# Kernel optimization log

Hardware: AMD Instinct MI355X
Metric: run time of the kernel (lower is better)

Reference implementation:

```python
import jax, jax.numpy as jnp
import numpy as np

N_SAMPLES = 16384
L = 8000   # num pseudo labels
C = 8      # num cameras
D = 256    # feature dim
N = 512    # batch size
T = 0.05   # temperature
K = 50     # hard_neg_k
LW = 0.5   # inter-cam loss weight


def setup_inputs() -> dict:
    key = jax.random.key(0)
    k1, k2, k3, k4, k5 = jax.random.split(key, 5)
    feats = jax.random.normal(k1, (N, D), dtype=jnp.float32)
    indexes = jax.random.randint(k2, (N,), 0, N_SAMPLES)
    label_table = jax.random.randint(k3, (N_SAMPLES,), 0, L)
    cam_table = jax.random.randint(k4, (N_SAMPLES,), 0, C)
    centers = jax.random.normal(k5, (L * C, D), dtype=jnp.float32)
    centers = centers / jnp.linalg.norm(centers, axis=1, keepdims=True)
    return {"feats": feats, "indexes": indexes, "label_table": label_table,
            "cam_table": cam_table, "centers": centers}


def reference(feats, indexes, label_table, cam_table, centers):
    # F.normalize(feats, p=2, dim=1)
    feats = feats / jnp.linalg.norm(feats, axis=1, keepdims=True)
    labels = label_table[indexes]          # [n]
    cams = cam_table[indexes]              # [n]
    cen = jax.lax.stop_gradient(centers)   # centers are a non-grad buffer in torch

    all_sims = feats @ cen.T               # [n, P]  P = L*C, proxy(l,c) = l*C + c
    n, P = all_sims.shape
    sims_r = all_sims.reshape(n, L, C)     # [n, L, C]

    # ---- intra-camera loss: softmax over the L proxies sharing sample's camera ----
    idx_cam = jnp.broadcast_to(cams[:, None, None], (n, L, 1))
    sims_intra = jnp.take_along_axis(sims_r, idx_cam, axis=2)[..., 0]  # [n, L]
    logp_intra = jax.nn.log_softmax(sims_intra / T, axis=1)
    loss_intra_i = -jnp.take_along_axis(logp_intra, labels[:, None], axis=1)[:, 0]

    # ---- inter-camera loss: C positives (same label, all cams) + top-K hard negatives ----
    idx_lab = jnp.broadcast_to(labels[:, None, None], (n, 1, C))
    pos_sims = jnp.take_along_axis(sims_r, idx_lab, axis=1)[:, 0, :]   # [n, C]
    masked = jnp.where(jnp.arange(L)[None, :, None] == labels[:, None, None],
                       jnp.float32(-10000.0), sims_r).reshape(n, P)
    neg_sims, _ = jax.lax.top_k(masked, K)                             # [n, K]
    logits = jnp.concatenate([pos_sims, neg_sims], axis=1) / T         # [n, C+K]
    logp = jax.nn.log_softmax(logits, axis=1)
    loss_inter_i = -jnp.mean(logp[:, :C], axis=1)  # target = 1/C on the C positives

    # ---- per-camera mean, summed over cameras (matches the torch.unique loop) ----
    ones = jnp.ones((n,), feats.dtype)
    counts = jax.ops.segment_sum(ones, cams, num_segments=C)
    safe = jnp.maximum(counts, 1.0)
    s_intra = jax.ops.segment_sum(loss_intra_i, cams, num_segments=C)
    s_inter = jax.ops.segment_sum(loss_inter_i, cams, num_segments=C)
    loss_intra = jnp.sum(jnp.where(counts > 0, s_intra / safe, 0.0))
    loss_inter = LW * jnp.sum(jnp.where(counts > 0, s_inter / safe, 0.0))
    return jnp.stack([loss_intra, loss_inter])
```

## Files before the change

kernel.cpp:

```cpp
#include <hip/hip_runtime.h>
#include <stdint.h>

#define NS   512
#define DDIM 256
#define LL   8000
#define CC   8
#define PP   64000
#define KTOP 50
#define CAP  1024
#define BC   64
#define NBLK (PP/BC)
#define K2C  28.853900817779268f

typedef float f32x4 __attribute__((ext_vector_type(4)));
typedef short bf16x8 __attribute__((ext_vector_type(8)));

__device__ __forceinline__ ushort f2bf(float x) {
    uint32_t b = __float_as_uint(x);
    b += 0x7fffu + ((b >> 16) & 1u);
    return (ushort)(b >> 16);
}
__device__ __forceinline__ float bf2f(ushort u) {
    return __uint_as_float(((uint32_t)u) << 16);
}

__global__ void k_norm_gather(const float* __restrict__ feats,
                              const int* __restrict__ indexes,
                              const int* __restrict__ ltab,
                              const int* __restrict__ ctab,
                              ushort* __restrict__ feats_b,
                              int* __restrict__ labels,
                              int* __restrict__ cams,
                              int* __restrict__ gcount) {
    const int n = blockIdx.x;
    const int lane = threadIdx.x;
    f32x4 v = ((const f32x4*)(feats + (size_t)n * DDIM))[lane];
    float ss = v[0]*v[0] + v[1]*v[1] + v[2]*v[2] + v[3]*v[3];
#pragma unroll
    for (int off = 32; off > 0; off >>= 1) ss += __shfl_down(ss, off);
    float tot = __shfl(ss, 0);
    float sc = 1.0f / sqrtf(tot);
    ushort4 o;
    o.x = f2bf(v[0] * sc); o.y = f2bf(v[1] * sc);
    o.z = f2bf(v[2] * sc); o.w = f2bf(v[3] * sc);
    ((ushort4*)(feats_b + (size_t)n * DDIM))[lane] = o;
    if (lane == 0) {
        int idx = indexes[n];
        labels[n] = ltab[idx];
        cams[n] = ctab[idx];
        gcount[n] = 0;
    }
}

__global__ __launch_bounds__(256, 2)
void k_gemm_fused(const ushort* __restrict__ A, const float* __restrict__ B,
                  const int* __restrict__ labels, const int* __restrict__ cams,
                  float* __restrict__ partial, float* __restrict__ cand,
                  int* __restrict__ gcount, float* __restrict__ posbuf) {
    const int bx    = blockIdx.x;
    const int cBase = bx * BC;
    const int gBase = cBase >> 3;
    const int tid   = threadIdx.x;
    const int lane  = tid & 63;
    const int w     = tid >> 6;
    const int lr    = lane & 15;
    const int lk    = lane >> 4;

    __shared__ ushort sB[BC][264];
    __shared__ int    s_lab[NS];
    __shared__ int    s_cam[NS];
    __shared__ float  s_intra[NS];
    __shared__ float  s_redA[256];
    __shared__ float  s_redB[256];
    __shared__ float  s_tau;

#pragma unroll
    for (int it = 0; it < 16; ++it) {
        int q   = tid + it * 256;
        int col = q >> 6;
        int k4  = q & 63;
        f32x4 a = *(const f32x4*)(B + (size_t)(cBase + col) * DDIM + k4 * 4);
        ushort4 o;
        o.x = f2bf(a[0]); o.y = f2bf(a[1]); o.z = f2bf(a[2]); o.w = f2bf(a[3]);
        *(ushort4*)(&sB[col][k4 * 4]) = o;
    }
    for (int r = tid; r < NS; r += 256) {
        s_lab[r] = labels[r];
        s_cam[r] = cams[r];
        s_intra[r] = 0.0f;
    }
    __syncthreads();

    const ushort* Abase = A + (size_t)(w * 128) * DDIM;
    bf16x8 acur[8];
#pragma unroll
    for (int m = 0; m < 8; ++m)
        acur[m] = *(const bf16x8*)(Abase + (size_t)(m * 16 + lr) * DDIM + lk * 8);

    f32x4 zero = {0.f, 0.f, 0.f, 0.f};
    f32x4 acc[8][4];
#pragma unroll
    for (int m = 0; m < 8; ++m)
#pragma unroll
        for (int nn = 0; nn < 4; ++nn) acc[m][nn] = zero;

#pragma unroll
    for (int kb = 0; kb < 8; ++kb) {
        const int kpos = kb * 32 + lk * 8;
        bf16x8 bfr[4];
#pragma unroll
        for (int nn = 0; nn < 4; ++nn)
            bfr[nn] = *(const bf16x8*)(&sB[nn * 16 + lr][kpos]);
        bf16x8 anxt[8];
        if (kb < 7) {
#pragma unroll
            for (int m = 0; m < 8; ++m)
                anxt[m] = *(const bf16x8*)(Abase + (size_t)(m * 16 + lr) * DDIM + kpos + 32);
        }
#pragma unroll
        for (int m = 0; m < 8; ++m)
#pragma unroll
            for (int nn = 0; nn < 4; ++nn)
                acc[m][nn] = __builtin_amdgcn_mfma_f32_16x16x32_bf16(acur[m], bfr[nn], acc[m][nn], 0, 0, 0);
        if (kb < 7) {
#pragma unroll
            for (int m = 0; m < 8; ++m) acur[m] = anxt[m];
        }
    }

    float ss = 0.0f, sc2 = 0.0f;
#pragma unroll
    for (int m = 0; m < 8; ++m)
#pragma unroll
        for (int nn = 0; nn < 4; ++nn)
#pragma unroll
            for (int j = 0; j < 4; ++j) {
                float v = acc[m][nn][j];
                if (fabsf(v) < 0.25f) { ss += v * v; sc2 += 1.0f; }
            }
    s_redA[tid] = ss; s_redB[tid] = sc2;
    __syncthreads();
    for (int off = 128; off > 0; off >>= 1) {
        if (tid < off) { s_redA[tid] += s_redA[tid + off]; s_redB[tid] += s_redB[tid + off]; }
        __syncthreads();
    }
    if (tid == 0) s_tau = 2.9f * sqrtf(s_redA[0] / fmaxf(s_redB[0], 1.0f));
    __syncthreads();
    const float tau = s_tau;

#pragma unroll
    for (int m = 0; m < 8; ++m) {
#pragma unroll
        for (int j = 0; j < 4; ++j) {
            const int r   = w * 128 + m * 16 + lk * 4 + j;
            const int lab = s_lab[r];
            const int cm  = s_cam[r];
            const bool mycam  = ((lr & 7) == cm);
            const bool hasLab = ((unsigned)(lab - gBase) < 8u);
            float isum = 0.0f;
#pragma unroll
            for (int nn = 0; nn < 4; ++nn) {
                const float v = acc[m][nn][j];
                if (mycam) isum += exp2f(v * K2C);
                const int g = gBase + ((nn * 16 + lr) >> 3);
                if (hasLab && g == lab) {
                    posbuf[r * CC + (lr & 7)] = v;
                } else if (v > tau) {
                    int id = atomicAdd(&gcount[r], 1);
                    if (id < CAP) cand[(size_t)r * CAP + id] = v;
                }
            }
            if (mycam) atomicAdd(&s_intra[r], isum);
        }
    }
    __syncthreads();
    for (int r = tid; r < NS; r += 256)
        partial[(size_t)bx * NS + r] = s_intra[r];
}

__global__ __launch_bounds__(256)
void k_row(const ushort* __restrict__ fb, const float* __restrict__ B,
           const float* __restrict__ partial, const float* __restrict__ cand,
           const int* __restrict__ gcount, const float* __restrict__ posbuf,
           const int* __restrict__ labels, const int* __restrict__ cams,
           float* __restrict__ li, float* __restrict__ le) {
    const int n = blockIdx.x;
    const int tid = threadIdx.x;
    __shared__ float red[256];
    __shared__ int   redi[256];
    __shared__ float spos[CC];
    __shared__ float scand[CAP];
    __shared__ float f[DDIM];
    __shared__ float s_lo, s_hi;
    __shared__ int   s_done, s_cnt;

    float s = 0.0f;
    for (int b = tid; b < NBLK; b += 256) s += partial[(size_t)b * NS + n];
    red[tid] = s;
    __syncthreads();
    for (int off = 128; off > 0; off >>= 1) {
        if (tid < off) red[tid] += red[tid + off];
        __syncthreads();
    }
    if (tid < CC) spos[tid] = posbuf[n * CC + tid];
    __syncthreads();
    if (tid == 0) li[n] = logf(red[0]) - 20.0f * spos[cams[n]];

    int c = gcount[n];
    if (c >= KTOP && c <= CAP) {
        for (int i = tid; i < c; i += 256) scand[i] = cand[(size_t)n * CAP + i];
    } else {
        if (tid < DDIM) f[tid] = bf2f(fb[(size_t)n * DDIM + tid]);
        const int label = labels[n];
        if (tid == 0) { s_lo = -1.01f; s_hi = 1.01f; s_done = 0; s_cnt = 0; }
        __syncthreads();
        for (int it = 0; it < 16; ++it) {
            if (s_done) break;
            float tm = 0.5f * (s_lo + s_hi);
            int cnt = 0;
            for (int p = tid; p < PP; p += 256) {
                if ((p >> 3) == label) continue;
                const float* col = B + (size_t)p * DDIM;
                float d = 0.0f;
                for (int k = 0; k < DDIM; ++k) d += f[k] * bf2f(f2bf(col[k]));
                cnt += (d > tm);
            }
            redi[tid] = cnt;
            __syncthreads();
            for (int off = 128; off > 0; off >>= 1) {
                if (tid < off) redi[tid] += redi[tid + off];
                __syncthreads();
            }
            int tot = redi[0];
            __syncthreads();
            if (tot >= KTOP && tot <= CAP) {
                if (tid == 0) s_cnt = 0;
                __syncthreads();
                for (int p = tid; p < PP; p += 256) {
                    if ((p >> 3) == label) continue;
                    const float* col = B + (size_t)p * DDIM;
                    float d = 0.0f;
                    for (int k = 0; k < DDIM; ++k) d += f[k] * bf2f(f2bf(col[k]));
                    if (d > tm) {
                        int id = atomicAdd(&s_cnt, 1);
                        if (id < CAP) scand[id] = d;
                    }
                }
                __syncthreads();
                if (tid == 0) s_done = 1;
            } else {
                if (tid == 0) { if (tot < KTOP) s_hi = tm; else s_lo = tm; }
            }
            __syncthreads();
        }
        if (!s_done) {
            if (tid == 0) s_cnt = 0;
            __syncthreads();
            float tl = s_lo;
            for (int p = tid; p < PP; p += 256) {
                if ((p >> 3) == label) continue;
                const float* col = B + (size_t)p * DDIM;
                float d = 0.0f;
                for (int k = 0; k < DDIM; ++k) d += f[k] * bf2f(f2bf(col[k]));
                if (d > tl) {
                    int id = atomicAdd(&s_cnt, 1);
                    if (id < CAP) scand[id] = d;
                }
            }
        }
        __syncthreads();
        c = s_cnt;
        if (c > CAP) c = CAP;
    }
    __syncthreads();

    float sum = 0.0f;
    for (int i = tid; i < c; i += 256) {
        float v = scand[i];
        int rk = 0;
        for (int j = 0; j < c; ++j) {
            float u = scand[j];
            rk += (u > v) || (u == v && j < i);
        }
        if (rk < KTOP) sum += exp2f(v * K2C);
    }
    if (tid < CC) sum += exp2f(spos[tid] * K2C);
    red[tid] = sum;
    __syncthreads();
    for (int off = 128; off > 0; off >>= 1) {
        if (tid < off) red[tid] += red[tid + off];
        __syncthreads();
    }
    if (tid == 0) {
        float ps = 0.0f;
#pragma unroll
        for (int j = 0; j < CC; ++j) ps += spos[j];
        le[n] = logf(red[0]) - 2.5f * ps;
    }
}

__global__ void k_finalize(const float* __restrict__ li, const float* __restrict__ le,
                           const int* __restrict__ cams, float* __restrict__ out) {
    __shared__ float si[CC], se[CC];
    __shared__ int sc[CC];
    int tid = threadIdx.x;
    if (tid < CC) { si[tid] = 0.f; se[tid] = 0.f; sc[tid] = 0; }
    __syncthreads();
    for (int i = tid; i < NS; i += 256) {
        int cm = cams[i];
        atomicAdd(&si[cm], li[i]);
        atomicAdd(&se[cm], le[i]);
        atomicAdd(&sc[cm], 1);
    }
    __syncthreads();
    if (tid == 0) {
        float a = 0.f, b = 0.f;
        for (int cm = 0; cm < CC; ++cm) {
            if (sc[cm] > 0) {
                a += si[cm] / (float)sc[cm];
                b += se[cm] / (float)sc[cm];
            }
        }
        out[0] = a;
        out[1] = 0.5f * b;
    }
}

extern "C" void kernel_launch(void* const* d_in, const int* in_sizes, int n_in,
                              void* d_out, int out_size, void* d_ws, size_t ws_size,
                              hipStream_t stream) {
    const float* feats   = (const float*)d_in[0];
    const int*   indexes = (const int*)d_in[1];
    const int*   ltab    = (const int*)d_in[2];
    const int*   ctab    = (const int*)d_in[3];
    const float* centers = (const float*)d_in[4];
    float* out = (float*)d_out;

    char* p = (char*)d_ws;
    float*  cand    = (float*)p;   p += (size_t)NS * CAP * sizeof(float);
    float*  partial = (float*)p;   p += (size_t)NBLK * NS * sizeof(float);
    float*  posbuf  = (float*)p;   p += (size_t)NS * CC * sizeof(float);
    ushort* fb      = (ushort*)p;  p += (size_t)NS * DDIM * sizeof(ushort);
    int*    labels  = (int*)p;     p += 2048;
    int*    cams    = (int*)p;     p += 2048;
    float*  li      = (float*)p;   p += 2048;
    float*  le      = (float*)p;   p += 2048;
    int*    gcount  = (int*)p;     p += 2048;

    hipLaunchKernelGGL(k_norm_gather, dim3(NS), dim3(64), 0, stream,
                       feats, indexes, ltab, ctab, fb, labels, cams, gcount);
    hipLaunchKernelGGL(k_gemm_fused, dim3(NBLK), dim3(256), 0, stream,
                       fb, centers, labels, cams, partial, cand, gcount, posbuf);
    hipLaunchKernelGGL(k_row, dim3(NS), dim3(256), 0, stream,
                       fb, centers, partial, cand, gcount, posbuf, labels, cams, li, le);
    hipLaunchKernelGGL(k_finalize, dim3(1), dim3(256), 0, stream, li, le, cams, out);
}
```

Measured before the change: 218.3 us.

## Retile fused GEMM into 128x128 2D tiles with LDS-staged A and streamed B

The fused similarity GEMM moves from column-strip blocks (all 512 rows × 64 proxies, A read from global into registers) to a 2D grid of 128×128 tiles. The A tile is staged once in LDS, and B is converted to bf16 and streamed through LDS one 32-wide k-slice at a time, with two barriers per step. The tau reduction now uses wavefront shuffles instead of a shared-memory tree. The aim is more blocks, fewer registers and less per-block LDS. The cost is that each proxy center row is read from global memory by four row-tile blocks instead of one, and the per-k-step barriers serialize loads with MFMA work.

```diff
diff --git a/kernel.cpp b/kernel.cpp
--- a/kernel.cpp
+++ b/kernel.cpp
@@ -8,8 +8,9 @@
 #define PP   64000
 #define KTOP 50
 #define CAP  1024
-#define BC   64
-#define NBLK (PP/BC)
+#define BM   128
+#define BN   128
+#define NCT  (PP/BN)
 #define K2C  28.853900817779268f
 
 typedef float f32x4 __attribute__((ext_vector_type(4)));
@@ -57,80 +58,89 @@
                   const int* __restrict__ labels, const int* __restrict__ cams,
                   float* __restrict__ partial, float* __restrict__ cand,
                   int* __restrict__ gcount, float* __restrict__ posbuf) {
-    const int bx    = blockIdx.x;
-    const int cBase = bx * BC;
-    const int gBase = cBase >> 3;
-    const int tid   = threadIdx.x;
-    const int lane  = tid & 63;
-    const int w     = tid >> 6;
-    const int lr    = lane & 15;
-    const int lk    = lane >> 4;
-
-    __shared__ ushort sB[BC][264];
-    __shared__ int    s_lab[NS];
-    __shared__ int    s_cam[NS];
-    __shared__ float  s_intra[NS];
-    __shared__ float  s_redA[256];
-    __shared__ float  s_redB[256];
+    const int ct = blockIdx.x;
+    const int rt = blockIdx.y;
+    const int C0 = ct * BN;
+    const int R0 = rt * BM;
+    const int tid  = threadIdx.x;
+    const int lane = tid & 63;
+    const int w    = tid >> 6;
+    const int wm   = w >> 1;
+    const int wn   = w & 1;
+    const int lr   = lane & 15;
+    const int lk   = lane >> 4;
+
+    __shared__ ushort sA[BM][264];
+    __shared__ ushort sB[BN][36];
+    __shared__ int    s_lab[BM];
+    __shared__ int    s_cam[BM];
+    __shared__ float  s_intra[BM];
+    __shared__ float  s_wred[8];
     __shared__ float  s_tau;
 
 #pragma unroll
     for (int it = 0; it < 16; ++it) {
         int q   = tid + it * 256;
-        int col = q >> 6;
-        int k4  = q & 63;
-        f32x4 a = *(const f32x4*)(B + (size_t)(cBase + col) * DDIM + k4 * 4);
-        ushort4 o;
-        o.x = f2bf(a[0]); o.y = f2bf(a[1]); o.z = f2bf(a[2]); o.w = f2bf(a[3]);
+        int row = q >> 5;
+        int c16 = q & 31;
+        *(bf16x8*)(&sA[row][c16 * 8]) =
+            *(const bf16x8*)(A + (size_t)(R0 + row) * DDIM + c16 * 8);
+    }
+    if (tid < BM) {
+        s_lab[tid] = labels[R0 + tid];
+        s_cam[tid] = cams[R0 + tid];
+        s_intra[tid] = 0.0f;
+    }
+
+#pragma unroll
+    for (int it = 0; it < 4; ++it) {
+        int q   = tid + it * 256;
+        int col = q >> 3;
+        int k4  = q & 7;
+        f32x4 v = *(const f32x4*)(B + (size_t)(C0 + col) * DDIM + k4 * 4);
+        ushort4 o = { f2bf(v[0]), f2bf(v[1]), f2bf(v[2]), f2bf(v[3]) };
         *(ushort4*)(&sB[col][k4 * 4]) = o;
     }
-    for (int r = tid; r < NS; r += 256) {
-        s_lab[r] = labels[r];
-        s_cam[r] = cams[r];
-        s_intra[r] = 0.0f;
-    }
-    __syncthreads();
-
-    const ushort* Abase = A + (size_t)(w * 128) * DDIM;
-    bf16x8 acur[8];
-#pragma unroll
-    for (int m = 0; m < 8; ++m)
-        acur[m] = *(const bf16x8*)(Abase + (size_t)(m * 16 + lr) * DDIM + lk * 8);
+    __syncthreads();
 
     f32x4 zero = {0.f, 0.f, 0.f, 0.f};
-    f32x4 acc[8][4];
-#pragma unroll
-    for (int m = 0; m < 8; ++m)
+    f32x4 acc[4][4];
+#pragma unroll
+    for (int m = 0; m < 4; ++m)
 #pragma unroll
         for (int nn = 0; nn < 4; ++nn) acc[m][nn] = zero;
 
-#pragma unroll
-    for (int kb = 0; kb < 8; ++kb) {
-        const int kpos = kb * 32 + lk * 8;
-        bf16x8 bfr[4];
+    for (int ks = 0; ks < 8; ++ks) {
+        bf16x8 af[4], bf[4];
+#pragma unroll
+        for (int m = 0; m < 4; ++m)
+            af[m] = *(const bf16x8*)(&sA[wm * 64 + m * 16 + lr][ks * 32 + lk * 8]);
 #pragma unroll
         for (int nn = 0; nn < 4; ++nn)
-            bfr[nn] = *(const bf16x8*)(&sB[nn * 16 + lr][kpos]);
-        bf16x8 anxt[8];
-        if (kb < 7) {
-#pragma unroll
-            for (int m = 0; m < 8; ++m)
-                anxt[m] = *(const bf16x8*)(Abase + (size_t)(m * 16 + lr) * DDIM + kpos + 32);
-        }
-#pragma unroll
-        for (int m = 0; m < 8; ++m)
+            bf[nn] = *(const bf16x8*)(&sB[wn * 64 + nn * 16 + lr][lk * 8]);
+#pragma unroll
+        for (int m = 0; m < 4; ++m)
 #pragma unroll
             for (int nn = 0; nn < 4; ++nn)
-                acc[m][nn] = __builtin_amdgcn_mfma_f32_16x16x32_bf16(acur[m], bfr[nn], acc[m][nn], 0, 0, 0);
-        if (kb < 7) {
-#pragma unroll
-            for (int m = 0; m < 8; ++m) acur[m] = anxt[m];
+                acc[m][nn] = __builtin_amdgcn_mfma_f32_16x16x32_bf16(af[m], bf[nn], acc[m][nn], 0, 0, 0);
+        if (ks < 7) {
+            __syncthreads();
+#pragma unroll
+            for (int it = 0; it < 4; ++it) {
+                int q   = tid + it * 256;
+                int col = q >> 3;
+                int k4  = q & 7;
+                f32x4 v = *(const f32x4*)(B + (size_t)(C0 + col) * DDIM + (ks + 1) * 32 + k4 * 4);
+                ushort4 o = { f2bf(v[0]), f2bf(v[1]), f2bf(v[2]), f2bf(v[3]) };
+                *(ushort4*)(&sB[col][k4 * 4]) = o;
+            }
+            __syncthreads();
         }
     }
 
     float ss = 0.0f, sc2 = 0.0f;
 #pragma unroll
-    for (int m = 0; m < 8; ++m)
+    for (int m = 0; m < 4; ++m)
 #pragma unroll
         for (int nn = 0; nn < 4; ++nn)
 #pragma unroll
@@ -138,44 +148,49 @@
                 float v = acc[m][nn][j];
                 if (fabsf(v) < 0.25f) { ss += v * v; sc2 += 1.0f; }
             }
-    s_redA[tid] = ss; s_redB[tid] = sc2;
-    __syncthreads();
-    for (int off = 128; off > 0; off >>= 1) {
-        if (tid < off) { s_redA[tid] += s_redA[tid + off]; s_redB[tid] += s_redB[tid + off]; }
-        __syncthreads();
-    }
-    if (tid == 0) s_tau = 2.9f * sqrtf(s_redA[0] / fmaxf(s_redB[0], 1.0f));
+#pragma unroll
+    for (int off = 32; off > 0; off >>= 1) {
+        ss  += __shfl_down(ss, off);
+        sc2 += __shfl_down(sc2, off);
+    }
+    if (lane == 0) { s_wred[w] = ss; s_wred[4 + w] = sc2; }
+    __syncthreads();
+    if (tid == 0) {
+        float S = s_wred[0] + s_wred[1] + s_wred[2] + s_wred[3];
+        float C = s_wred[4] + s_wred[5] + s_wred[6] + s_wred[7];
+        s_tau = 2.9f * sqrtf(S / fmaxf(C, 1.0f));
+    }
     __syncthreads();
     const float tau = s_tau;
 
 #pragma unroll
-    for (int m = 0; m < 8; ++m) {
+    for (int m = 0; m < 4; ++m) {
 #pragma unroll
         for (int j = 0; j < 4; ++j) {
-            const int r   = w * 128 + m * 16 + lk * 4 + j;
-            const int lab = s_lab[r];
-            const int cm  = s_cam[r];
-            const bool mycam  = ((lr & 7) == cm);
-            const bool hasLab = ((unsigned)(lab - gBase) < 8u);
+            const int rl  = wm * 64 + m * 16 + lk * 4 + j;
+            const int r   = R0 + rl;
+            const int lab = s_lab[rl];
+            const int cm  = s_cam[rl];
+            const bool mycam = ((lr & 7) == cm);
             float isum = 0.0f;
 #pragma unroll
             for (int nn = 0; nn < 4; ++nn) {
+                const int c_loc = wn * 64 + nn * 16 + lr;
                 const float v = acc[m][nn][j];
                 if (mycam) isum += exp2f(v * K2C);
-                const int g = gBase + ((nn * 16 + lr) >> 3);
-                if (hasLab && g == lab) {
-                    posbuf[r * CC + (lr & 7)] = v;
+                const int g = (C0 + c_loc) >> 3;
+                if (g == lab) {
+                    posbuf[r * CC + (c_loc & 7)] = v;
                 } else if (v > tau) {
                     int id = atomicAdd(&gcount[r], 1);
                     if (id < CAP) cand[(size_t)r * CAP + id] = v;
                 }
             }
-            if (mycam) atomicAdd(&s_intra[r], isum);
-        }
-    }
-    __syncthreads();
-    for (int r = tid; r < NS; r += 256)
-        partial[(size_t)bx * NS + r] = s_intra[r];
+            if (mycam) atomicAdd(&s_intra[rl], isum);
+        }
+    }
+    __syncthreads();
+    if (tid < BM) partial[(size_t)ct * NS + R0 + tid] = s_intra[tid];
 }
 
 __global__ __launch_bounds__(256)
@@ -195,7 +210,7 @@
     __shared__ int   s_done, s_cnt;
 
     float s = 0.0f;
-    for (int b = tid; b < NBLK; b += 256) s += partial[(size_t)b * NS + n];
+    for (int b = tid; b < NCT; b += 256) s += partial[(size_t)b * NS + n];
     red[tid] = s;
     __syncthreads();
     for (int off = 128; off > 0; off >>= 1) {
@@ -338,7 +353,7 @@
 
     char* p = (char*)d_ws;
     float*  cand    = (float*)p;   p += (size_t)NS * CAP * sizeof(float);
-    float*  partial = (float*)p;   p += (size_t)NBLK * NS * sizeof(float);
+    float*  partial = (float*)p;   p += (size_t)NCT * NS * sizeof(float);
     float*  posbuf  = (float*)p;   p += (size_t)NS * CC * sizeof(float);
     ushort* fb      = (ushort*)p;  p += (size_t)NS * DDIM * sizeof(ushort);
     int*    labels  = (int*)p;     p += 2048;
@@ -349,7 +364,7 @@
 
     hipLaunchKernelGGL(k_norm_gather, dim3(NS), dim3(64), 0, stream,
                        feats, indexes, ltab, ctab, fb, labels, cams, gcount);
-    hipLaunchKernelGGL(k_gemm_fused, dim3(NBLK), dim3(256), 0, stream,
+    hipLaunchKernelGGL(k_gemm_fused, dim3(NCT, 4), dim3(256), 0, stream,
                        fb, centers, labels, cams, partial, cand, gcount, posbuf);
     hipLaunchKernelGGL(k_row, dim3(NS), dim3(256), 0, stream,
                        fb, centers, partial, cand, gcount, posbuf, labels, cams, li, le);
```

Result: slower. 238.1 us (+9.1%).
